# Optimization experiments

Hardware: AMD Instinct MI355X
Metric: run time of the kernel (lower is better)

Reference implementation:

```python
import jax, jax.numpy as jnp
from jax import lax
import numpy as np
import math

IMG_H, IMG_W = 592, 800  # stride-16 image for a 50x37 feature map


def _make_anchors(fx=50, fy=37, base=8, dsr=16):
    rows = []
    for x in range(fx):
        for y in range(fy):
            for size in [base, 2 * base, 4 * base]:
                rows.append([(x - size / 2) * dsr, (y - size / 2) * dsr,
                             (x + size / 2) * dsr, (y + size / 2) * dsr])
                s = math.sqrt(size ** 2 / 2)
                rows.append([(x - s) * dsr, (y - s / 2) * dsr, (x + s) * dsr, (y + s / 2) * dsr])
                rows.append([(x - s / 2) * dsr, (y - s) * dsr, (x + s / 2) * dsr, (y + s) * dsr])
    return np.array(rows, np.float32)


def setup_inputs() -> dict:
    key = jax.random.key(0)
    k = jax.random.split(key, 8)
    B, G, H, W = 32, 20, 50, 37
    feats = jax.random.normal(k[0], (B, 512, H, W), jnp.float32)
    a = _make_anchors()
    keep = (a[:, 0] >= 0) & (a[:, 1] >= 0) & (a[:, 2] <= IMG_W) & (a[:, 3] <= IMG_H)
    idxs_inside = jnp.asarray(np.nonzero(keep)[0].astype(np.int32))
    anchors = jnp.asarray(a[keep])
    # valid xyxy GT boxes inside the image
    x1 = jax.random.uniform(k[1], (B, G)) * (IMG_W - 160)
    y1 = jax.random.uniform(k[2], (B, G)) * (IMG_H - 160)
    w = 32.0 + jax.random.uniform(k[3], (B, G)) * 96.0
    h = 32.0 + jax.random.uniform(k[4], (B, G)) * 96.0
    gt_boxes = jnp.stack([x1, y1, x1 + w, y1 + h], -1)
    W3 = jax.random.normal(k[5], (512, 512, 3, 3), jnp.float32) * 0.02
    b3 = jnp.zeros((512,), jnp.float32)
    Wcls = jax.random.normal(k[6], (18, 512, 1, 1), jnp.float32) * 0.02
    bcls = jnp.zeros((18,), jnp.float32)
    Wloc = jax.random.normal(k[7], (36, 512, 1, 1), jnp.float32) * 0.02
    bloc = jnp.zeros((36,), jnp.float32)
    return {"feats": feats, "gt_boxes": gt_boxes, "anchors": anchors,
            "W3": W3, "b3": b3, "Wcls": Wcls, "bcls": bcls,
            "Wloc": Wloc, "bloc": bloc, "idxs_inside": idxs_inside}


def _conv(x, w, b, pad):
    y = lax.conv_general_dilated(x, w, (1, 1), pad,
                                 dimension_numbers=("NCHW", "OIHW", "NCHW"))
    return y + b[None, :, None, None]


def reference(feats, gt_boxes, anchors, W3, b3, Wcls, bcls, Wloc, bloc, idxs_inside):
    B = feats.shape[0]
    rpn_conv1 = jax.nn.relu(_conv(feats, W3, b3, "SAME"))
    cls_score = _conv(rpn_conv1, Wcls, bcls, "VALID")          # [B,18,H,W]
    _, C, H, Wd = cls_score.shape
    logits = cls_score.reshape(B, 2, (C * H) // 2, Wd)          # reshape(x, 2)
    prob = jax.nn.softmax(logits, axis=1)
    prob_back = prob.reshape(B, C, H, Wd)                       # reshape back to 18
    loc_pred = _conv(rpn_conv1, Wloc, bloc, "VALID")            # [B,36,H,W]

    # select inside-image anchors
    logits_sel = logits.transpose(0, 2, 3, 1).reshape(B, -1, 2)[:, idxs_inside, :]
    loc_sel = loc_pred.transpose(0, 2, 3, 1).reshape(B, -1, 4)[:, idxs_inside, :]

    # vectorized anchors x gt IoU (replaces the triple python loop)
    ix1 = jnp.maximum(anchors[None, :, None, 0], gt_boxes[:, None, :, 0])
    iy1 = jnp.maximum(anchors[None, :, None, 1], gt_boxes[:, None, :, 1])
    ix2 = jnp.minimum(anchors[None, :, None, 2], gt_boxes[:, None, :, 2])
    iy2 = jnp.minimum(anchors[None, :, None, 3], gt_boxes[:, None, :, 3])
    inter = jnp.clip(ix2 - ix1, 0) * jnp.clip(iy2 - iy1, 0)     # [B,A,G]
    area_a = (anchors[:, 2] - anchors[:, 0]) * (anchors[:, 3] - anchors[:, 1])
    area_g = (gt_boxes[..., 2] - gt_boxes[..., 0]) * (gt_boxes[..., 3] - gt_boxes[..., 1])
    iou = inter / jnp.maximum(area_a[None, :, None] + area_g[:, None, :] - inter, 1e-8)

    max_iou = iou.max(-1)                                       # [B,A]
    matched = iou.argmax(-1)                                    # [B,A] gt index per anchor
    gt_best = iou.argmax(1)                                     # [B,G] best anchor per gt
    A = anchors.shape[0]
    is_best = jnp.zeros((B, A), bool).at[jnp.arange(B)[:, None], gt_best].set(True)
    labels = (is_best | (max_iou > 0.7)).astype(jnp.int32)      # positives=1, rest 0

    logsm = jax.nn.log_softmax(logits_sel, -1)
    loss_cls = -jnp.take_along_axis(logsm, labels[..., None], -1).mean()

    tgt = jnp.take_along_axis(gt_boxes, matched[:, :, None], axis=1)  # [B,A,4]
    d = loc_sel - tgt
    sl1 = jnp.where(jnp.abs(d) < 1.0, 0.5 * d * d, jnp.abs(d) - 0.5)
    loss_loc = (sl1 * labels[..., None].astype(sl1.dtype)).sum() / 256.0

    return prob_back, loc_pred, loss_cls, loss_loc
```

## Files before the change

kernel.cpp:

```cpp
#include <hip/hip_runtime.h>
#include <stdint.h>

typedef unsigned short u16;
typedef unsigned int   u32;
typedef unsigned long long u64;

typedef __bf16 v8bf __attribute__((ext_vector_type(8)));
typedef float  v4f  __attribute__((ext_vector_type(4)));

#define NBATCH 32
#define NCH    512
#define FH     50
#define FW     37
#define PIX    1850
#define MTOT   59200
#define KTOT   4608
#define HP     52
#define WP     39
#define NG     20

#define PROB_N 1065600
#define LOC_N  2131200
#define LC_IDX 3196800
#define LL_IDX 3196801

__device__ __forceinline__ u16 f2bf(float f) {
    u32 u = __float_as_uint(f);
    u += 0x7fffu + ((u >> 16) & 1u);
    return (u16)(u >> 16);
}
__device__ __forceinline__ float bf_lo(u32 u){ return __uint_as_float(u << 16); }
__device__ __forceinline__ float bf_hi(u32 u){ return __uint_as_float(u & 0xffff0000u); }

__device__ __forceinline__ void gl_lds16(const u16* g, u16* l) {
    __builtin_amdgcn_global_load_lds((const __attribute__((address_space(1))) u32*)g,
                                     (__attribute__((address_space(3))) u32*)l,
                                     16, 0, 0);
}

__global__ __launch_bounds__(256) void pad_kernel(const float* __restrict__ feats,
                                                  u16* __restrict__ fpad) {
    __shared__ float t[64][65];
    const int b  = blockIdx.z;
    const int c0 = blockIdx.y * 64;
    const int p0 = blockIdx.x * 64;
    const int tid = threadIdx.x;
    {
        const int cl = tid >> 2, seg = tid & 3;
        const float* src = feats + ((size_t)b * NCH + c0 + cl) * PIX;
        const int pbase = p0 + seg * 16;
        #pragma unroll
        for (int i = 0; i < 16; i++) {
            int p = pbase + i;
            t[cl][seg * 16 + i] = (p < PIX) ? src[p] : 0.f;
        }
    }
    __syncthreads();
    {
        const int pl = tid >> 2, cs = tid & 3;
        const int p = p0 + pl;
        if (p < PIX) {
            const int h = p / FW, w = p % FW;
            size_t dst = (((size_t)b * HP + h + 1) * WP + (w + 1)) * NCH + c0 + cs * 16;
            u32 pk[8];
            #pragma unroll
            for (int i = 0; i < 8; i++) {
                u32 lo = f2bf(t[cs * 16 + 2 * i][pl]);
                u32 hi = f2bf(t[cs * 16 + 2 * i + 1][pl]);
                pk[i] = lo | (hi << 16);
            }
            *(uint4*)&fpad[dst]     = make_uint4(pk[0], pk[1], pk[2], pk[3]);
            *(uint4*)&fpad[dst + 8] = make_uint4(pk[4], pk[5], pk[6], pk[7]);
        }
    }
}

__global__ void wprep3(const float* __restrict__ w3, u16* __restrict__ wbt) {
    int t = blockIdx.x * 256 + threadIdx.x;
    if (t < NCH * KTOT) {
        int co = t / KTOT, k = t % KTOT;
        int dydx = k >> 9, ci = k & 511;
        wbt[t] = f2bf(w3[((size_t)co * NCH + ci) * 9 + dydx]);
    }
}

__global__ void wprep1(const float* __restrict__ wcls, const float* __restrict__ wloc,
                       u16* __restrict__ wcb) {
    int t = blockIdx.x * 256 + threadIdx.x;
    if (t < 54 * 512) {
        int c = t >> 9, ci = t & 511;
        float v = (c < 18) ? wcls[c * 512 + ci] : wloc[(c - 18) * 512 + ci];
        wcb[t] = f2bf(v);
    }
}

__global__ __launch_bounds__(256) void conv3x3_mfma(const u16* __restrict__ fpad,
                                                    const u16* __restrict__ wbt,
                                                    const float* __restrict__ b3,
                                                    u16* __restrict__ conv1) {
    __shared__ __align__(16) u16 As[128][32];
    __shared__ __align__(16) u16 Bs[128][32];

    const int tid = threadIdx.x;
    const int m_base = blockIdx.x * 128;
    const int n_base = blockIdx.y * 128;

    const int row = tid >> 2;
    const int seg = tid & 3;
    const int wave = tid >> 6;
    const int lane = tid & 63;

    int rb[2];
    #pragma unroll
    for (int r = 0; r < 2; r++) {
        int m = m_base + row + r * 64;
        int mm = (m < MTOT) ? m : 0;
        int b = mm / PIX;
        int p = mm % PIX;
        int y = p / FW;
        int x = p % FW;
        rb[r] = ((b * HP + y) * WP + x) * NCH;
    }
    int wbrow[2];
    #pragma unroll
    for (int r = 0; r < 2; r++) {
        int n = n_base + row + r * 64;
        wbrow[r] = n * KTOT + seg * 8;
    }

    u16* const as0 = &As[0][0] + wave * 512;
    u16* const as1 = &As[0][0] + 2048 + wave * 512;
    u16* const bs0 = &Bs[0][0] + wave * 512;
    u16* const bs1 = &Bs[0][0] + 2048 + wave * 512;

    const int wm = (wave >> 1) * 64;
    const int wn = (wave & 1) * 64;
    const int lm = lane & 15;
    const int quad = lane >> 4;
    const int q8 = quad * 8;

    v4f acc[4][4];
    #pragma unroll
    for (int i = 0; i < 4; i++)
        #pragma unroll
        for (int j = 0; j < 4; j++)
            #pragma unroll
            for (int r = 0; r < 4; r++) acc[i][j][r] = 0.f;

    for (int k0 = 0; k0 < KTOT; k0 += 32) {
        const int dydx = k0 >> 9;
        const int ci0  = k0 & 511;
        const int offA = ((dydx / 3) * WP + (dydx % 3)) * NCH + ci0 + seg * 8;
        gl_lds16(fpad + rb[0] + offA, as0);
        gl_lds16(fpad + rb[1] + offA, as1);
        gl_lds16(wbt + wbrow[0] + k0, bs0);
        gl_lds16(wbt + wbrow[1] + k0, bs1);
        __syncthreads();

        v8bf af[4], bfv[4];
        #pragma unroll
        for (int i = 0; i < 4; i++) af[i]  = *(const v8bf*)&As[wm + i * 16 + lm][q8];
        #pragma unroll
        for (int i = 0; i < 4; i++) bfv[i] = *(const v8bf*)&Bs[wn + i * 16 + lm][q8];
        #pragma unroll
        for (int i = 0; i < 4; i++)
            #pragma unroll
            for (int j = 0; j < 4; j++)
                acc[i][j] = __builtin_amdgcn_mfma_f32_16x16x32_bf16(af[i], bfv[j], acc[i][j], 0, 0, 0);
        __syncthreads();
    }

    #pragma unroll
    for (int j = 0; j < 4; j++) {
        const int n = n_base + wn + j * 16 + lm;
        const float bias = b3[n];
        #pragma unroll
        for (int i = 0; i < 4; i++) {
            #pragma unroll
            for (int r = 0; r < 4; r++) {
                int m = m_base + wm + i * 16 + quad * 4 + r;
                if (m < MTOT) {
                    float v = acc[i][j][r] + bias;
                    v = v > 0.f ? v : 0.f;
                    conv1[(size_t)m * NCH + n] = f2bf(v);
                }
            }
        }
    }
}

__global__ __launch_bounds__(256) void head_kernel(const u16* __restrict__ conv1,
                                                   const u16* __restrict__ wcb,
                                                   const float* __restrict__ bcls,
                                                   const float* __restrict__ bloc,
                                                   float* __restrict__ out) {
    __shared__ __align__(16) u16 xl[4][520];
    __shared__ float cls_l[4][18];
    const int tid = threadIdx.x;
    const int m0 = blockIdx.x * 4;
    {
        const int r = tid & 3;
        const int kk = (tid >> 2) * 8;
        *(uint4*)&xl[r][kk] = *(const uint4*)&conv1[(size_t)(m0 + r) * NCH + kk];
    }
    __syncthreads();
    const int c = tid >> 2;
    const int pix = tid & 3;
    float a0 = 0.f, a1 = 0.f, a2 = 0.f, a3 = 0.f;
    if (c < 54) {
        const uint4* wp = (const uint4*)(wcb + c * 512);
        #pragma unroll 8
        for (int it = 0; it < 64; it++) {
            uint4 xv = *(const uint4*)&xl[pix][it * 8];
            uint4 wv = wp[it];
            a0 = fmaf(bf_lo(xv.x), bf_lo(wv.x), a0);
            a1 = fmaf(bf_hi(xv.x), bf_hi(wv.x), a1);
            a2 = fmaf(bf_lo(xv.y), bf_lo(wv.y), a2);
            a3 = fmaf(bf_hi(xv.y), bf_hi(wv.y), a3);
            a0 = fmaf(bf_lo(xv.z), bf_lo(wv.z), a0);
            a1 = fmaf(bf_hi(xv.z), bf_hi(wv.z), a1);
            a2 = fmaf(bf_lo(xv.w), bf_lo(wv.w), a2);
            a3 = fmaf(bf_hi(xv.w), bf_hi(wv.w), a3);
        }
    }
    float acc = (a0 + a1) + (a2 + a3);
    const int m = m0 + pix;
    const int b = m / PIX;
    const int p = m % PIX;
    if (c >= 18 && c < 54) {
        out[(size_t)PROB_N + ((size_t)b * 36 + (c - 18)) * PIX + p] = acc + bloc[c - 18];
    }
    if (c < 18) cls_l[pix][c] = acc + bcls[c];
    __syncthreads();
    if (c < 9) {
        float s0 = cls_l[pix][c], s1 = cls_l[pix][c + 9];
        float mx = fmaxf(s0, s1);
        float e0 = expf(s0 - mx), e1 = expf(s1 - mx);
        float inv = 1.f / (e0 + e1);
        out[((size_t)b * 18 + c) * PIX + p]     = e0 * inv;
        out[((size_t)b * 18 + c + 9) * PIX + p] = e1 * inv;
    }
}

__global__ __launch_bounds__(256) void iou_kernel(const float* __restrict__ anchors,
                                                  const float* __restrict__ gtb,
                                                  int A,
                                                  float* __restrict__ max_iou,
                                                  int* __restrict__ matched,
                                                  u64* __restrict__ gtkey) {
    __shared__ float g[NG * 4];
    __shared__ u64 wk[4][NG];
    const int b = blockIdx.y;
    const int tid = threadIdx.x;
    if (tid < NG * 4) g[tid] = gtb[b * NG * 4 + tid];
    __syncthreads();
    const int a = blockIdx.x * 256 + tid;
    const bool act = a < A;
    const int aa = act ? a : 0;
    const float ax1 = anchors[aa * 4 + 0], ay1 = anchors[aa * 4 + 1];
    const float ax2 = anchors[aa * 4 + 2], ay2 = anchors[aa * 4 + 3];
    const float areaA = (ax2 - ax1) * (ay2 - ay1);
    float best = -1.f;
    int bg = 0;
    const int lane = tid & 63, wave = tid >> 6;
    for (int gi = 0; gi < NG; gi++) {
        float gx1 = g[gi * 4], gy1 = g[gi * 4 + 1], gx2 = g[gi * 4 + 2], gy2 = g[gi * 4 + 3];
        float iw = fmaxf(fminf(ax2, gx2) - fmaxf(ax1, gx1), 0.f);
        float ih = fmaxf(fminf(ay2, gy2) - fmaxf(ay1, gy1), 0.f);
        float inter = iw * ih;
        float areaG = (gx2 - gx1) * (gy2 - gy1);
        float iou = inter / fmaxf(areaA + areaG - inter, 1e-8f);
        if (act && iou > best) { best = iou; bg = gi; }
        u64 key = act ? (((u64)__float_as_uint(iou) << 32) | (u64)(0xFFFFFFFFu - (u32)a)) : 0ull;
        #pragma unroll
        for (int off = 32; off; off >>= 1) {
            u64 o = __shfl_xor(key, off);
            key = (o > key) ? o : key;
        }
        if (lane == 0) wk[wave][gi] = key;
    }
    if (act) {
        max_iou[(size_t)b * A + a] = best;
        matched[(size_t)b * A + a] = bg;
    }
    __syncthreads();
    if (tid < NG) {
        u64 k = wk[0][tid];
        k = (wk[1][tid] > k) ? wk[1][tid] : k;
        k = (wk[2][tid] > k) ? wk[2][tid] : k;
        k = (wk[3][tid] > k) ? wk[3][tid] : k;
        atomicMax(&gtkey[b * NG + tid], k);
    }
}

__global__ __launch_bounds__(256) void loss_kernel(const float* __restrict__ gtb,
                                                   const int* __restrict__ idxs,
                                                   const float* __restrict__ max_iou,
                                                   const int* __restrict__ matched,
                                                   const u64* __restrict__ gtkey,
                                                   int A,
                                                   float* out) {
    __shared__ float g[NG * 4];
    __shared__ int gbest[NG];
    __shared__ float red[8];
    const int b = blockIdx.y;
    const int tid = threadIdx.x;
    if (tid < NG * 4) g[tid] = gtb[b * NG * 4 + tid];
    if (tid < NG) {
        u64 k = gtkey[b * NG + tid];
        gbest[tid] = (int)(0xFFFFFFFFu - (u32)(k & 0xFFFFFFFFull));
    }
    __syncthreads();
    const int a = blockIdx.x * 256 + tid;
    float lc = 0.f, ll = 0.f;
    if (a < A) {
        float mi = max_iou[(size_t)b * A + a];
        int lbl = (mi > 0.7f) ? 1 : 0;
        if (!lbl) {
            #pragma unroll
            for (int gi = 0; gi < NG; gi++) lbl |= (gbest[gi] == a);
        }
        const int idx = idxs[a];
        const int cpr = idx / PIX;
        const int rem = idx % PIX;
        float p0 = out[((size_t)b * 18 + cpr) * PIX + rem];
        float p1 = out[((size_t)b * 18 + cpr + 9) * PIX + rem];
        float pl = lbl ? p1 : p0;
        lc = -logf(pl);
        if (lbl) {
            const int mg = matched[(size_t)b * A + a];
            const int hh = idx / 333;
            const int r2 = idx % 333;
            const int ww = r2 / 9;
            const int c4 = r2 % 9;
            const int pp = hh * FW + ww;
            #pragma unroll
            for (int t = 0; t < 4; t++) {
                float lv = out[(size_t)PROB_N + ((size_t)b * 36 + c4 * 4 + t) * PIX + pp];
                float d = lv - g[mg * 4 + t];
                float ad = fabsf(d);
                ll += (ad < 1.f) ? 0.5f * d * d : ad - 0.5f;
            }
        }
    }
    #pragma unroll
    for (int off = 32; off; off >>= 1) {
        lc += __shfl_xor(lc, off);
        ll += __shfl_xor(ll, off);
    }
    const int lane = tid & 63, wave = tid >> 6;
    if (lane == 0) { red[wave] = lc; red[4 + wave] = ll; }
    __syncthreads();
    if (tid == 0) {
        float slc = red[0] + red[1] + red[2] + red[3];
        float sll = red[4] + red[5] + red[6] + red[7];
        atomicAdd(&out[LC_IDX], slc * (1.f / (32.f * (float)A)));
        atomicAdd(&out[LL_IDX], sll * (1.f / 256.f));
    }
}

extern "C" void kernel_launch(void* const* d_in, const int* in_sizes, int n_in,
                              void* d_out, int out_size, void* d_ws, size_t ws_size,
                              hipStream_t stream) {
    const float* feats   = (const float*)d_in[0];
    const float* gtb     = (const float*)d_in[1];
    const float* anchors = (const float*)d_in[2];
    const float* W3      = (const float*)d_in[3];
    const float* b3      = (const float*)d_in[4];
    const float* Wcls    = (const float*)d_in[5];
    const float* bcls    = (const float*)d_in[6];
    const float* Wloc    = (const float*)d_in[7];
    const float* bloc    = (const float*)d_in[8];
    const int*   idxs    = (const int*)d_in[9];
    const int A = in_sizes[9];
    float* out = (float*)d_out;

    char* ws = (char*)d_ws;
    size_t off = 0;
    auto alloc = [&](size_t bytes) -> void* {
        void* p = ws + off;
        off = (off + bytes + 255) & ~(size_t)255;
        return p;
    };
    const size_t fpad_n = (size_t)NBATCH * HP * WP * NCH;
    u16* fpad   = (u16*)alloc(fpad_n * 2);
    u16* wbt    = (u16*)alloc((size_t)NCH * KTOT * 2);
    u16* wcb    = (u16*)alloc((size_t)54 * 512 * 2);
    u16* conv1  = (u16*)alloc((size_t)MTOT * NCH * 2);
    u64* gtkey  = (u64*)alloc((size_t)NBATCH * NG * 8);
    float* max_iou = (float*)alloc((size_t)NBATCH * A * 4);
    int*   matched = (int*)alloc((size_t)NBATCH * A * 4);

    hipMemsetAsync(fpad, 0, fpad_n * 2, stream);
    hipMemsetAsync(gtkey, 0, (size_t)NBATCH * NG * 8, stream);
    hipMemsetAsync(out + LC_IDX, 0, 8, stream);

    pad_kernel<<<dim3(29, 8, NBATCH), 256, 0, stream>>>(feats, fpad);
    wprep3<<<(NCH * KTOT + 255) / 256, 256, 0, stream>>>(W3, wbt);
    wprep1<<<(54 * 512 + 255) / 256, 256, 0, stream>>>(Wcls, Wloc, wcb);
    conv3x3_mfma<<<dim3(463, 4), 256, 0, stream>>>(fpad, wbt, b3, conv1);
    head_kernel<<<MTOT / 4, 256, 0, stream>>>(conv1, wcb, bcls, bloc, out);
    const int ablk = (A + 255) / 256;
    iou_kernel<<<dim3(ablk, NBATCH), 256, 0, stream>>>(anchors, gtb, A, max_iou, matched, gtkey);
    loss_kernel<<<dim3(ablk, NBATCH), 256, 0, stream>>>(gtb, idxs, max_iou, matched, gtkey, A, out);
}
```

Before: 912.9 us.

## Double conv K-tile to 64 with XOR-swizzled LDS, zero only pad border

```diff
diff --git a/kernel.cpp b/kernel.cpp
--- a/kernel.cpp
+++ b/kernel.cpp
@@ -18,6 +18,7 @@
 #define HP     52
 #define WP     39
 #define NG     20
+#define W3N    (NCH*KTOT)
 
 #define PROB_N 1065600
 #define LOC_N  2131200
@@ -75,22 +76,35 @@
     }
 }
 
-__global__ void wprep3(const float* __restrict__ w3, u16* __restrict__ wbt) {
+__global__ __launch_bounds__(256) void border_kernel(u16* __restrict__ fpad) {
     int t = blockIdx.x * 256 + threadIdx.x;
-    if (t < NCH * KTOT) {
+    int c8 = t & 63;
+    int pi = (t >> 6) % 178;
+    int b  = (t >> 6) / 178;
+    int h, w;
+    if (pi < 39)       { h = 0;        w = pi; }
+    else if (pi < 78)  { h = 51;       w = pi - 39; }
+    else if (pi < 128) { h = pi - 77;  w = 0; }
+    else               { h = pi - 127; w = 38; }
+    size_t dst = (((size_t)b * HP + h) * WP + w) * NCH + c8 * 8;
+    *(uint4*)&fpad[dst] = make_uint4(0, 0, 0, 0);
+}
+
+__global__ void wprep(const float* __restrict__ w3, const float* __restrict__ wcls,
+                      const float* __restrict__ wloc,
+                      u16* __restrict__ wbt, u16* __restrict__ wcb) {
+    int t = blockIdx.x * 256 + threadIdx.x;
+    if (t < W3N) {
         int co = t / KTOT, k = t % KTOT;
         int dydx = k >> 9, ci = k & 511;
         wbt[t] = f2bf(w3[((size_t)co * NCH + ci) * 9 + dydx]);
-    }
-}
-
-__global__ void wprep1(const float* __restrict__ wcls, const float* __restrict__ wloc,
-                       u16* __restrict__ wcb) {
-    int t = blockIdx.x * 256 + threadIdx.x;
-    if (t < 54 * 512) {
-        int c = t >> 9, ci = t & 511;
-        float v = (c < 18) ? wcls[c * 512 + ci] : wloc[(c - 18) * 512 + ci];
-        wcb[t] = f2bf(v);
+    } else {
+        int t2 = t - W3N;
+        if (t2 < 54 * 512) {
+            int c = t2 >> 9, ci = t2 & 511;
+            float v = (c < 18) ? wcls[c * 512 + ci] : wloc[(c - 18) * 512 + ci];
+            wcb[t2] = f2bf(v);
+        }
     }
 }
 
@@ -98,46 +112,42 @@
                                                     const u16* __restrict__ wbt,
                                                     const float* __restrict__ b3,
                                                     u16* __restrict__ conv1) {
-    __shared__ __align__(16) u16 As[128][32];
-    __shared__ __align__(16) u16 Bs[128][32];
+    __shared__ __align__(16) u16 As[128][64];
+    __shared__ __align__(16) u16 Bs[128][64];
 
     const int tid = threadIdx.x;
     const int m_base = blockIdx.x * 128;
     const int n_base = blockIdx.y * 128;
-
-    const int row = tid >> 2;
-    const int seg = tid & 3;
     const int wave = tid >> 6;
     const int lane = tid & 63;
 
-    int rb[2];
+    const int srow  = tid >> 3;
+    const int seg_g = (tid & 7) ^ (srow & 7);
+
+    int rbA[4];
     #pragma unroll
-    for (int r = 0; r < 2; r++) {
-        int m = m_base + row + r * 64;
+    for (int r = 0; r < 4; r++) {
+        int m = m_base + r * 32 + srow;
         int mm = (m < MTOT) ? m : 0;
-        int b = mm / PIX;
-        int p = mm % PIX;
-        int y = p / FW;
-        int x = p % FW;
-        rb[r] = ((b * HP + y) * WP + x) * NCH;
-    }
-    int wbrow[2];
+        int b = mm / PIX, p = mm % PIX;
+        int y = p / FW, x = p % FW;
+        rbA[r] = ((b * HP + y) * WP + x) * NCH + seg_g * 8;
+    }
+    int rbB[4];
     #pragma unroll
-    for (int r = 0; r < 2; r++) {
-        int n = n_base + row + r * 64;
-        wbrow[r] = n * KTOT + seg * 8;
-    }
-
-    u16* const as0 = &As[0][0] + wave * 512;
-    u16* const as1 = &As[0][0] + 2048 + wave * 512;
-    u16* const bs0 = &Bs[0][0] + wave * 512;
-    u16* const bs1 = &Bs[0][0] + 2048 + wave * 512;
+    for (int r = 0; r < 4; r++) {
+        int n = n_base + r * 32 + srow;
+        rbB[r] = n * KTOT + seg_g * 8;
+    }
+
+    u16* const asb = &As[0][0] + wave * 512;
+    u16* const bsb = &Bs[0][0] + wave * 512;
 
     const int wm = (wave >> 1) * 64;
     const int wn = (wave & 1) * 64;
     const int lm = lane & 15;
     const int quad = lane >> 4;
-    const int q8 = quad * 8;
+    const int x7 = lm & 7;
 
     v4f acc[4][4];
     #pragma unroll
@@ -147,26 +157,34 @@
             #pragma unroll
             for (int r = 0; r < 4; r++) acc[i][j][r] = 0.f;
 
-    for (int k0 = 0; k0 < KTOT; k0 += 32) {
+    for (int k0 = 0; k0 < KTOT; k0 += 64) {
         const int dydx = k0 >> 9;
         const int ci0  = k0 & 511;
-        const int offA = ((dydx / 3) * WP + (dydx % 3)) * NCH + ci0 + seg * 8;
-        gl_lds16(fpad + rb[0] + offA, as0);
-        gl_lds16(fpad + rb[1] + offA, as1);
-        gl_lds16(wbt + wbrow[0] + k0, bs0);
-        gl_lds16(wbt + wbrow[1] + k0, bs1);
+        const int offA = ((dydx / 3) * WP + (dydx % 3)) * NCH + ci0;
+        #pragma unroll
+        for (int r = 0; r < 4; r++)
+            gl_lds16(fpad + rbA[r] + offA, asb + r * 2048);
+        #pragma unroll
+        for (int r = 0; r < 4; r++)
+            gl_lds16(wbt + rbB[r] + k0, bsb + r * 2048);
         __syncthreads();
 
-        v8bf af[4], bfv[4];
-        #pragma unroll
-        for (int i = 0; i < 4; i++) af[i]  = *(const v8bf*)&As[wm + i * 16 + lm][q8];
-        #pragma unroll
-        for (int i = 0; i < 4; i++) bfv[i] = *(const v8bf*)&Bs[wn + i * 16 + lm][q8];
-        #pragma unroll
-        for (int i = 0; i < 4; i++)
-            #pragma unroll
-            for (int j = 0; j < 4; j++)
-                acc[i][j] = __builtin_amdgcn_mfma_f32_16x16x32_bf16(af[i], bfv[j], acc[i][j], 0, 0, 0);
+        #pragma unroll
+        for (int kh = 0; kh < 2; kh++) {
+            const int ps = (((kh << 2) | quad) ^ x7) * 8;
+            v8bf af[4], bfv[4];
+            #pragma unroll
+            for (int i = 0; i < 4; i++)
+                af[i]  = *(const v8bf*)(&As[0][0] + (wm + i * 16 + lm) * 64 + ps);
+            #pragma unroll
+            for (int i = 0; i < 4; i++)
+                bfv[i] = *(const v8bf*)(&Bs[0][0] + (wn + i * 16 + lm) * 64 + ps);
+            #pragma unroll
+            for (int i = 0; i < 4; i++)
+                #pragma unroll
+                for (int j = 0; j < 4; j++)
+                    acc[i][j] = __builtin_amdgcn_mfma_f32_16x16x32_bf16(af[i], bfv[j], acc[i][j], 0, 0, 0);
+        }
         __syncthreads();
     }
 
@@ -391,13 +409,12 @@
     float* max_iou = (float*)alloc((size_t)NBATCH * A * 4);
     int*   matched = (int*)alloc((size_t)NBATCH * A * 4);
 
-    hipMemsetAsync(fpad, 0, fpad_n * 2, stream);
     hipMemsetAsync(gtkey, 0, (size_t)NBATCH * NG * 8, stream);
     hipMemsetAsync(out + LC_IDX, 0, 8, stream);
 
+    border_kernel<<<1424, 256, 0, stream>>>(fpad);
     pad_kernel<<<dim3(29, 8, NBATCH), 256, 0, stream>>>(feats, fpad);
-    wprep3<<<(NCH * KTOT + 255) / 256, 256, 0, stream>>>(W3, wbt);
-    wprep1<<<(54 * 512 + 255) / 256, 256, 0, stream>>>(Wcls, Wloc, wcb);
+    wprep<<<(W3N + 54 * 512 + 255) / 256, 256, 0, stream>>>(W3, Wcls, Wloc, wbt, wcb);
     conv3x3_mfma<<<dim3(463, 4), 256, 0, stream>>>(fpad, wbt, b3, conv1);
     head_kernel<<<MTOT / 4, 256, 0, stream>>>(conv1, wcb, bcls, bloc, out);
     const int ablk = (A + 255) / 256;
```

After: 886.3 us. 1.03x faster.
